# Kernel tuning notes

Measured on AMD Instinct MI355X. Metric: run time of the kernel, lower is better.

The kernel has to match this reference:

```python
import jax, jax.numpy as jnp
import numpy as np

B, V, D, H, E = 512, 128, 256, 4, 2
Dh = D // H

def setup_inputs() -> dict:
    key = jax.random.key(0)
    k = jax.random.split(key, 8)
    x = jax.random.normal(k[0], (B, V, D), dtype=jnp.float32)
    adj = jax.random.randint(k[1], (V, V), 0, 2, dtype=jnp.int32)
    adj = adj.at[jnp.arange(V), jnp.arange(V)].set(1)  # self loops so no empty columns for real nodes
    edge_attr = jax.random.normal(k[2], (V, V, E), dtype=jnp.float32)
    mask = jax.random.bernoulli(k[3], 0.1, (B, V))  # True = padded view
    # learned params (torch Linear: y = x @ W.T)
    W = jax.random.normal(k[4], (D, D), dtype=jnp.float32) / np.sqrt(D)
    a = jax.random.normal(k[5], (2 * Dh,), dtype=jnp.float32) / np.sqrt(2 * Dh)  # attn.weight flattened
    Ew = jax.random.normal(k[6], (H, E), dtype=jnp.float32) / np.sqrt(E)  # edge_proj.weight
    return {"x": x, "adj": adj, "edge_attr": edge_attr, "mask": mask, "W": W, "a": a, "Ew": Ew}

def reference(x, adj, edge_attr, mask, W, a, Ew):
    Bv, Vv, Dv = x.shape
    Hh = Ew.shape[0]
    Dhh = Dv // Hh
    Wx = (x @ W.T).reshape(Bv, Vv, Hh, Dhh)                 # [B,V,H,Dh]
    a_src, a_dst = a[:Dhh], a[Dhh:]
    s_src = jnp.einsum('bvhd,d->bvh', Wx, a_src)             # a^T[Wh_i ; .]
    s_dst = jnp.einsum('bvhd,d->bvh', Wx, a_dst)             # a^T[. ; Wh_j]
    ef = jnp.einsum('ije,he->ijh', edge_attr, Ew)            # [V,V,H]
    e = s_src[:, :, None, :] + s_dst[:, None, :, :] + ef[None]  # [B,i,j,H]
    e = jnp.where(e >= 0, e, 0.2 * e)                        # leaky_relu(0.2)
    valid = (adj.astype(bool))[None, :, :, None] & (~mask)[:, :, None, None] & (~mask)[:, None, :, None]
    e = jnp.where(valid, e, -jnp.inf)
    # softmax over source dim i (axis=1), safe for all-masked columns (-> 0, like nan_to_num)
    m = jnp.max(e, axis=1, keepdims=True)
    m = jnp.where(jnp.isfinite(m), m, 0.0)
    p = jnp.where(valid, jnp.exp(e - m), 0.0)
    denom = jnp.sum(p, axis=1, keepdims=True)
    alpha = p / jnp.where(denom == 0, 1.0, denom)            # [B,i,j,H]
    h = jnp.einsum('bijh,bihd->bjhd', alpha, Wx).reshape(Bv, Vv, Dv)
    h = jax.nn.elu(h)
    return jnp.where(mask[:, :, None], 0.0, h)
```

## Files before the change

### kernel.cpp

```cpp
#include <hip/hip_runtime.h>
#include <hip/hip_bf16.h>
#include <cmath>

#define BB 512
#define VV 128
#define DD 256
#define HH 4
#define DHH 64

typedef unsigned short u16;
typedef __attribute__((ext_vector_type(8))) short bf16x8;
typedef __attribute__((ext_vector_type(4))) float f32x4;

__device__ __forceinline__ unsigned pk2(float a, float b) {
    __hip_bfloat162 h = __float22bfloat162_rn(make_float2(a, b));
    unsigned r;
    __builtin_memcpy(&r, &h, sizeof(r));
    return r;
}

__global__ __launch_bounds__(256) void k_ef(const float* __restrict__ ea,
                                            const float* __restrict__ Ew,
                                            const int* __restrict__ adj,
                                            float* __restrict__ efmT) {
    __shared__ float tile[32][33];
    const int jt = blockIdx.x, it = blockIdx.y, h = blockIdx.z;
    const int t = threadIdx.x;
    const float e0 = Ew[h * 2], e1 = Ew[h * 2 + 1];
    const int jl = t & 31, il = t >> 5;
    #pragma unroll
    for (int p = 0; p < 4; ++p) {
        const int i = it * 32 + p * 8 + il;
        const int j = jt * 32 + jl;
        const int ij = i * VV + j;
        float v = -INFINITY;
        if (adj[ij]) v = fmaf(ea[ij * 2 + 1], e1, ea[ij * 2] * e0);
        tile[p * 8 + il][jl] = v;
    }
    __syncthreads();
    const int i2 = t & 31, j2 = t >> 5;
    #pragma unroll
    for (int p = 0; p < 4; ++p) {
        const int j = p * 8 + j2;
        efmT[((size_t)h * VV + jt * 32 + j) * VV + it * 32 + i2] = tile[i2][j];
    }
}

__global__ __launch_bounds__(256, 3) void k_fused(
    const float* __restrict__ x, const float* __restrict__ Wm,
    const float* __restrict__ a, const float* __restrict__ efmT,
    const int* __restrict__ mask, float* __restrict__ out) {
    __shared__ u16 WxL[128 * 136];
    __shared__ float ssl[256], sdl[256], rden[2][128];

    const int t = threadIdx.x;
    const int b = blockIdx.x, hp = blockIdx.y;
    const int w = t >> 6, L = t & 63;
    const int wr = w >> 1, wc = w & 1;
    const int lr = L & 15, lg = L >> 4;

    const float* xb = x  + ((size_t)b * VV + wr * 64 + lr) * DD + lg * 8;
    const float* wb = Wm + ((size_t)(hp * 128 + wc * 64 + lr)) * DD + lg * 8;

    f32x4 acc[4][4];
    #pragma unroll
    for (int i = 0; i < 4; ++i)
        #pragma unroll
        for (int j = 0; j < 4; ++j) acc[i][j] = (f32x4){0.f, 0.f, 0.f, 0.f};

    for (int ks = 0; ks < 8; ++ks) {
        float4 la[4][2], lb[4][2];
        #pragma unroll
        for (int f = 0; f < 4; ++f) {
            la[f][0] = *(const float4*)(xb + (size_t)f * 16 * DD + ks * 32);
            la[f][1] = *(const float4*)(xb + (size_t)f * 16 * DD + ks * 32 + 4);
        }
        #pragma unroll
        for (int f = 0; f < 4; ++f) {
            lb[f][0] = *(const float4*)(wb + (size_t)f * 16 * DD + ks * 32);
            lb[f][1] = *(const float4*)(wb + (size_t)f * 16 * DD + ks * 32 + 4);
        }
        bf16x8 af[4], bf[4];
        #pragma unroll
        for (int f = 0; f < 4; ++f) {
            unsigned* u = (unsigned*)&af[f];
            u[0] = pk2(la[f][0].x, la[f][0].y); u[1] = pk2(la[f][0].z, la[f][0].w);
            u[2] = pk2(la[f][1].x, la[f][1].y); u[3] = pk2(la[f][1].z, la[f][1].w);
            unsigned* v = (unsigned*)&bf[f];
            v[0] = pk2(lb[f][0].x, lb[f][0].y); v[1] = pk2(lb[f][0].z, lb[f][0].w);
            v[2] = pk2(lb[f][1].x, lb[f][1].y); v[3] = pk2(lb[f][1].z, lb[f][1].w);
        }
        #pragma unroll
        for (int mi = 0; mi < 4; ++mi)
            #pragma unroll
            for (int ni = 0; ni < 4; ++ni)
                acc[mi][ni] = __builtin_amdgcn_mfma_f32_16x16x32_bf16(
                    af[mi], bf[ni], acc[mi][ni], 0, 0, 0);
    }

    float as_[4], ad_[4];
    #pragma unroll
    for (int ni = 0; ni < 4; ++ni) {
        as_[ni] = a[ni * 16 + lr];
        ad_[ni] = a[64 + ni * 16 + lr];
    }
    float ps[16], pd[16];
    #pragma unroll
    for (int k = 0; k < 16; ++k) { ps[k] = 0.f; pd[k] = 0.f; }
    #pragma unroll
    for (int mi = 0; mi < 4; ++mi) {
        #pragma unroll
        for (int ni = 0; ni < 4; ++ni) {
            const int c  = wc * 64 + ni * 16 + lr;
            const int vb = wr * 64 + mi * 16 + lg * 4;
            unsigned o2[2];
            o2[0] = pk2(acc[mi][ni][0], acc[mi][ni][1]);
            o2[1] = pk2(acc[mi][ni][2], acc[mi][ni][3]);
            #pragma unroll
            for (int r = 0; r < 4; ++r) {
                float v = acc[mi][ni][r];
                ps[mi * 4 + r] = fmaf(v, as_[ni], ps[mi * 4 + r]);
                pd[mi * 4 + r] = fmaf(v, ad_[ni], pd[mi * 4 + r]);
            }
            *(uint2*)&WxL[c * 136 + vb] = *(uint2*)&o2[0];
        }
    }
    #pragma unroll
    for (int k = 0; k < 16; ++k) {
        #pragma unroll
        for (int m = 1; m < 16; m <<= 1) {
            ps[k] += __shfl_xor(ps[k], m);
            pd[k] += __shfl_xor(pd[k], m);
        }
    }
    if (lr == 0) {
        #pragma unroll
        for (int mi = 0; mi < 4; ++mi)
            #pragma unroll
            for (int r = 0; r < 4; ++r) {
                int v = wr * 64 + mi * 16 + lg * 4 + r;
                bool mk = mask[b * VV + v] != 0;
                ssl[wc * 128 + v] = mk ? -INFINITY : ps[mi * 4 + r];
                sdl[wc * 128 + v] = mk ? -INFINITY : pd[mi * 4 + r];
            }
    }
    __syncthreads();

    const int j0 = w * 32 + lr;
    for (int hl = 0; hl < 2; ++hl) {
        const int h = hp * 2 + hl;
        const float sdj0 = sdl[hl * 128 + j0];
        const float sdj1 = sdl[hl * 128 + j0 + 16];
        const float* ef0 = efmT + ((size_t)h * VV + j0) * VV;
        const float* ef1 = ef0 + 16 * VV;
        bf16x8 af2[2][4];
        float ps0 = 0.f, ps1 = 0.f;
        #pragma unroll
        for (int ks = 0; ks < 4; ++ks) {
            const int i0 = ks * 32 + lg * 8;
            float sv[8], ev0[8], ev1[8];
            *(float4*)&sv[0]  = *(const float4*)&ssl[hl * 128 + i0];
            *(float4*)&sv[4]  = *(const float4*)&ssl[hl * 128 + i0 + 4];
            *(float4*)&ev0[0] = *(const float4*)(ef0 + i0);
            *(float4*)&ev0[4] = *(const float4*)(ef0 + i0 + 4);
            *(float4*)&ev1[0] = *(const float4*)(ef1 + i0);
            *(float4*)&ev1[4] = *(const float4*)(ef1 + i0 + 4);
            float p0[8], p1[8];
            #pragma unroll
            for (int u = 0; u < 8; ++u) {
                float e0 = sv[u] + sdj0 + ev0[u];
                float e1 = sv[u] + sdj1 + ev1[u];
                e0 = fmaxf(e0, 0.2f * e0);
                e1 = fmaxf(e1, 0.2f * e1);
                p0[u] = __expf(e0); ps0 += p0[u];
                p1[u] = __expf(e1); ps1 += p1[u];
            }
            unsigned* a0 = (unsigned*)&af2[0][ks];
            unsigned* a1 = (unsigned*)&af2[1][ks];
            a0[0] = pk2(p0[0], p0[1]); a0[1] = pk2(p0[2], p0[3]);
            a0[2] = pk2(p0[4], p0[5]); a0[3] = pk2(p0[6], p0[7]);
            a1[0] = pk2(p1[0], p1[1]); a1[1] = pk2(p1[2], p1[3]);
            a1[2] = pk2(p1[4], p1[5]); a1[3] = pk2(p1[6], p1[7]);
        }
        ps0 += __shfl_xor(ps0, 16); ps0 += __shfl_xor(ps0, 32);
        ps1 += __shfl_xor(ps1, 16); ps1 += __shfl_xor(ps1, 32);
        if (lg == 0) {
            rden[hl][j0]      = ps0 > 0.f ? 1.f / ps0 : 0.f;
            rden[hl][j0 + 16] = ps1 > 0.f ? 1.f / ps1 : 0.f;
        }

        f32x4 acc2[2][4];
        #pragma unroll
        for (int mi = 0; mi < 2; ++mi)
            #pragma unroll
            for (int ni = 0; ni < 4; ++ni) acc2[mi][ni] = (f32x4){0.f, 0.f, 0.f, 0.f};
        #pragma unroll
        for (int ks = 0; ks < 4; ++ks) {
            const int kk = ks * 32 + lg * 8;
            #pragma unroll
            for (int ni = 0; ni < 4; ++ni) {
                bf16x8 bf2 = *(const bf16x8*)&WxL[(hl * 64 + ni * 16 + lr) * 136 + kk];
                acc2[0][ni] = __builtin_amdgcn_mfma_f32_16x16x32_bf16(
                    af2[0][ks], bf2, acc2[0][ni], 0, 0, 0);
                acc2[1][ni] = __builtin_amdgcn_mfma_f32_16x16x32_bf16(
                    af2[1][ks], bf2, acc2[1][ni], 0, 0, 0);
            }
        }

        #pragma unroll
        for (int mi = 0; mi < 2; ++mi)
            #pragma unroll
            for (int ni = 0; ni < 4; ++ni) {
                const int dcol = ni * 16 + lr;
                const int jb   = w * 32 + mi * 16 + lg * 4;
                float* op = out + ((size_t)b * VV + jb) * DD + h * DHH + dcol;
                #pragma unroll
                for (int r = 0; r < 4; ++r) {
                    float v = acc2[mi][ni][r] * rden[hl][jb + r];
                    v = v > 0.f ? v : (__expf(v) - 1.0f);
                    op[(size_t)r * DD] = v;
                }
            }
    }
}

extern "C" void kernel_launch(void* const* d_in, const int* in_sizes, int n_in,
                              void* d_out, int out_size, void* d_ws, size_t ws_size,
                              hipStream_t stream) {
    const float* x    = (const float*)d_in[0];
    const int*   adj  = (const int*)d_in[1];
    const float* ea   = (const float*)d_in[2];
    const int*   mask = (const int*)d_in[3];
    const float* Wm   = (const float*)d_in[4];
    const float* a    = (const float*)d_in[5];
    const float* Ew   = (const float*)d_in[6];
    float* out = (float*)d_out;

    float* efmT = (float*)d_ws;

    k_ef<<<dim3(4, 4, HH), 256, 0, stream>>>(ea, Ew, adj, efmT);
    k_fused<<<dim3(BB, 2), 256, 0, stream>>>(x, Wm, a, efmT, mask, out);
}
```

Baseline: 182.8 us.

## Split fused GAT kernel per head and stage GEMM operands through LDS

```diff
diff --git a/kernel.cpp b/kernel.cpp
--- a/kernel.cpp
+++ b/kernel.cpp
@@ -46,56 +46,75 @@
     }
 }
 
-__global__ __launch_bounds__(256, 3) void k_fused(
+__global__ __launch_bounds__(256, 4) void k_fused(
     const float* __restrict__ x, const float* __restrict__ Wm,
     const float* __restrict__ a, const float* __restrict__ efmT,
     const int* __restrict__ mask, float* __restrict__ out) {
-    __shared__ u16 WxL[128 * 136];
-    __shared__ float ssl[256], sdl[256], rden[2][128];
+    __shared__ u16 ubuf[8704];
+    __shared__ float ssl[128], sdl[128], rden[128];
+
+    u16* As  = ubuf;
+    u16* Bs  = ubuf + 5120;
+    u16* WxL = ubuf;
 
     const int t = threadIdx.x;
-    const int b = blockIdx.x, hp = blockIdx.y;
+    const int h = blockIdx.x, b = blockIdx.y;
     const int w = t >> 6, L = t & 63;
-    const int wr = w >> 1, wc = w & 1;
     const int lr = L & 15, lg = L >> 4;
 
-    const float* xb = x  + ((size_t)b * VV + wr * 64 + lr) * DD + lg * 8;
-    const float* wb = Wm + ((size_t)(hp * 128 + wc * 64 + lr)) * DD + lg * 8;
-
-    f32x4 acc[4][4];
-    #pragma unroll
-    for (int i = 0; i < 4; ++i)
+    const int arow = t >> 1, aseg = t & 1;
+    const int brow = t >> 2, bseg = t & 3;
+    const float* xs = x  + ((size_t)b * VV + arow) * DD + aseg * 16;
+    const float* ws = Wm + ((size_t)(h * 64 + brow)) * DD + bseg * 8;
+    u16* adst = As + arow * 40 + aseg * 16;
+    u16* bdst = Bs + brow * 40 + bseg * 8;
+
+    f32x4 acc[2][4];
+    #pragma unroll
+    for (int i = 0; i < 2; ++i)
         #pragma unroll
         for (int j = 0; j < 4; ++j) acc[i][j] = (f32x4){0.f, 0.f, 0.f, 0.f};
 
+    float4 px[4], pw[2];
+    #pragma unroll
+    for (int q = 0; q < 4; ++q) px[q] = *(const float4*)(xs + q * 4);
+    #pragma unroll
+    for (int q = 0; q < 2; ++q) pw[q] = *(const float4*)(ws + q * 4);
+
     for (int ks = 0; ks < 8; ++ks) {
-        float4 la[4][2], lb[4][2];
-        #pragma unroll
-        for (int f = 0; f < 4; ++f) {
-            la[f][0] = *(const float4*)(xb + (size_t)f * 16 * DD + ks * 32);
-            la[f][1] = *(const float4*)(xb + (size_t)f * 16 * DD + ks * 32 + 4);
-        }
-        #pragma unroll
-        for (int f = 0; f < 4; ++f) {
-            lb[f][0] = *(const float4*)(wb + (size_t)f * 16 * DD + ks * 32);
-            lb[f][1] = *(const float4*)(wb + (size_t)f * 16 * DD + ks * 32 + 4);
-        }
-        bf16x8 af[4], bf[4];
-        #pragma unroll
-        for (int f = 0; f < 4; ++f) {
-            unsigned* u = (unsigned*)&af[f];
-            u[0] = pk2(la[f][0].x, la[f][0].y); u[1] = pk2(la[f][0].z, la[f][0].w);
-            u[2] = pk2(la[f][1].x, la[f][1].y); u[3] = pk2(la[f][1].z, la[f][1].w);
-            unsigned* v = (unsigned*)&bf[f];
-            v[0] = pk2(lb[f][0].x, lb[f][0].y); v[1] = pk2(lb[f][0].z, lb[f][0].w);
-            v[2] = pk2(lb[f][1].x, lb[f][1].y); v[3] = pk2(lb[f][1].z, lb[f][1].w);
-        }
-        #pragma unroll
-        for (int mi = 0; mi < 4; ++mi)
+        unsigned va[4], vb[4], qa[4];
+        va[0] = pk2(px[0].x, px[0].y); va[1] = pk2(px[0].z, px[0].w);
+        va[2] = pk2(px[1].x, px[1].y); va[3] = pk2(px[1].z, px[1].w);
+        vb[0] = pk2(px[2].x, px[2].y); vb[1] = pk2(px[2].z, px[2].w);
+        vb[2] = pk2(px[3].x, px[3].y); vb[3] = pk2(px[3].z, px[3].w);
+        qa[0] = pk2(pw[0].x, pw[0].y); qa[1] = pk2(pw[0].z, pw[0].w);
+        qa[2] = pk2(pw[1].x, pw[1].y); qa[3] = pk2(pw[1].z, pw[1].w);
+        *(bf16x8*)adst       = *(bf16x8*)&va[0];
+        *(bf16x8*)(adst + 8) = *(bf16x8*)&vb[0];
+        *(bf16x8*)bdst       = *(bf16x8*)&qa[0];
+        __syncthreads();
+        if (ks < 7) {
+            #pragma unroll
+            for (int q = 0; q < 4; ++q)
+                px[q] = *(const float4*)(xs + (ks + 1) * 32 + q * 4);
+            #pragma unroll
+            for (int q = 0; q < 2; ++q)
+                pw[q] = *(const float4*)(ws + (ks + 1) * 32 + q * 4);
+        }
+        bf16x8 af[2], bfr[4];
+        #pragma unroll
+        for (int mi = 0; mi < 2; ++mi)
+            af[mi] = *(const bf16x8*)&As[(w * 32 + mi * 16 + lr) * 40 + lg * 8];
+        #pragma unroll
+        for (int ni = 0; ni < 4; ++ni)
+            bfr[ni] = *(const bf16x8*)&Bs[(ni * 16 + lr) * 40 + lg * 8];
+        #pragma unroll
+        for (int mi = 0; mi < 2; ++mi)
             #pragma unroll
             for (int ni = 0; ni < 4; ++ni)
                 acc[mi][ni] = __builtin_amdgcn_mfma_f32_16x16x32_bf16(
-                    af[mi], bf[ni], acc[mi][ni], 0, 0, 0);
+                    af[mi], bfr[ni], acc[mi][ni], 0, 0, 0);
+        __syncthreads();
     }
 
     float as_[4], ad_[4];
@@ -104,15 +123,15 @@
         as_[ni] = a[ni * 16 + lr];
         ad_[ni] = a[64 + ni * 16 + lr];
     }
-    float ps[16], pd[16];
-    #pragma unroll
-    for (int k = 0; k < 16; ++k) { ps[k] = 0.f; pd[k] = 0.f; }
-    #pragma unroll
-    for (int mi = 0; mi < 4; ++mi) {
+    float ps[8], pd[8];
+    #pragma unroll
+    for (int k = 0; k < 8; ++k) { ps[k] = 0.f; pd[k] = 0.f; }
+    #pragma unroll
+    for (int mi = 0; mi < 2; ++mi) {
         #pragma unroll
         for (int ni = 0; ni < 4; ++ni) {
-            const int c  = wc * 64 + ni * 16 + lr;
-            const int vb = wr * 64 + mi * 16 + lg * 4;
+            const int c  = ni * 16 + lr;
+            const int vb = w * 32 + mi * 16 + lg * 4;
             unsigned o2[2];
             o2[0] = pk2(acc[mi][ni][0], acc[mi][ni][1]);
             o2[1] = pk2(acc[mi][ni][2], acc[mi][ni][3]);
@@ -126,7 +145,7 @@
         }
     }
     #pragma unroll
-    for (int k = 0; k < 16; ++k) {
+    for (int k = 0; k < 8; ++k) {
         #pragma unroll
         for (int m = 1; m < 16; m <<= 1) {
             ps[k] += __shfl_xor(ps[k], m);
@@ -135,93 +154,90 @@
     }
     if (lr == 0) {
         #pragma unroll
-        for (int mi = 0; mi < 4; ++mi)
+        for (int mi = 0; mi < 2; ++mi)
             #pragma unroll
             for (int r = 0; r < 4; ++r) {
-                int v = wr * 64 + mi * 16 + lg * 4 + r;
+                int v = w * 32 + mi * 16 + lg * 4 + r;
                 bool mk = mask[b * VV + v] != 0;
-                ssl[wc * 128 + v] = mk ? -INFINITY : ps[mi * 4 + r];
-                sdl[wc * 128 + v] = mk ? -INFINITY : pd[mi * 4 + r];
+                ssl[v] = mk ? -INFINITY : ps[mi * 4 + r];
+                sdl[v] = mk ? -INFINITY : pd[mi * 4 + r];
             }
     }
     __syncthreads();
 
     const int j0 = w * 32 + lr;
-    for (int hl = 0; hl < 2; ++hl) {
-        const int h = hp * 2 + hl;
-        const float sdj0 = sdl[hl * 128 + j0];
-        const float sdj1 = sdl[hl * 128 + j0 + 16];
-        const float* ef0 = efmT + ((size_t)h * VV + j0) * VV;
-        const float* ef1 = ef0 + 16 * VV;
-        bf16x8 af2[2][4];
-        float ps0 = 0.f, ps1 = 0.f;
-        #pragma unroll
-        for (int ks = 0; ks < 4; ++ks) {
-            const int i0 = ks * 32 + lg * 8;
-            float sv[8], ev0[8], ev1[8];
-            *(float4*)&sv[0]  = *(const float4*)&ssl[hl * 128 + i0];
-            *(float4*)&sv[4]  = *(const float4*)&ssl[hl * 128 + i0 + 4];
-            *(float4*)&ev0[0] = *(const float4*)(ef0 + i0);
-            *(float4*)&ev0[4] = *(const float4*)(ef0 + i0 + 4);
-            *(float4*)&ev1[0] = *(const float4*)(ef1 + i0);
-            *(float4*)&ev1[4] = *(const float4*)(ef1 + i0 + 4);
-            float p0[8], p1[8];
-            #pragma unroll
-            for (int u = 0; u < 8; ++u) {
-                float e0 = sv[u] + sdj0 + ev0[u];
-                float e1 = sv[u] + sdj1 + ev1[u];
-                e0 = fmaxf(e0, 0.2f * e0);
-                e1 = fmaxf(e1, 0.2f * e1);
-                p0[u] = __expf(e0); ps0 += p0[u];
-                p1[u] = __expf(e1); ps1 += p1[u];
+    const float sdj0 = sdl[j0];
+    const float sdj1 = sdl[j0 + 16];
+    const float* ef0 = efmT + ((size_t)h * VV + j0) * VV;
+    const float* ef1 = ef0 + 16 * VV;
+    bf16x8 af2[2][4];
+    float ps0 = 0.f, ps1 = 0.f;
+    #pragma unroll
+    for (int ks = 0; ks < 4; ++ks) {
+        const int i0 = ks * 32 + lg * 8;
+        float sv[8], ev0[8], ev1[8];
+        *(float4*)&sv[0]  = *(const float4*)&ssl[i0];
+        *(float4*)&sv[4]  = *(const float4*)&ssl[i0 + 4];
+        *(float4*)&ev0[0] = *(const float4*)(ef0 + i0);
+        *(float4*)&ev0[4] = *(const float4*)(ef0 + i0 + 4);
+        *(float4*)&ev1[0] = *(const float4*)(ef1 + i0);
+        *(float4*)&ev1[4] = *(const float4*)(ef1 + i0 + 4);
+        float p0[8], p1[8];
+        #pragma unroll
+        for (int u = 0; u < 8; ++u) {
+            float e0 = sv[u] + sdj0 + ev0[u];
+            float e1 = sv[u] + sdj1 + ev1[u];
+            e0 = fmaxf(e0, 0.2f * e0);
+            e1 = fmaxf(e1, 0.2f * e1);
+            p0[u] = __expf(e0); ps0 += p0[u];
+            p1[u] = __expf(e1); ps1 += p1[u];
+        }
+        unsigned* a0 = (unsigned*)&af2[0][ks];
+        unsigned* a1 = (unsigned*)&af2[1][ks];
+        a0[0] = pk2(p0[0], p0[1]); a0[1] = pk2(p0[2], p0[3]);
+        a0[2] = pk2(p0[4], p0[5]); a0[3] = pk2(p0[6], p0[7]);
+        a1[0] = pk2(p1[0], p1[1]); a1[1] = pk2(p1[2], p1[3]);
+        a1[2] = pk2(p1[4], p1[5]); a1[3] = pk2(p1[6], p1[7]);
+    }
+    ps0 += __shfl_xor(ps0, 16); ps0 += __shfl_xor(ps0, 32);
+    ps1 += __shfl_xor(ps1, 16); ps1 += __shfl_xor(ps1, 32);
+    if (lg == 0) {
+        rden[j0]      = ps0 > 0.f ? 1.f / ps0 : 0.f;
+        rden[j0 + 16] = ps1 > 0.f ? 1.f / ps1 : 0.f;
+    }
+
+    f32x4 acc2[2][4];
+    #pragma unroll
+    for (int mi = 0; mi < 2; ++mi)
+        #pragma unroll
+        for (int ni = 0; ni < 4; ++ni) acc2[mi][ni] = (f32x4){0.f, 0.f, 0.f, 0.f};
+    #pragma unroll
+    for (int ks = 0; ks < 4; ++ks) {
+        const int kk = ks * 32 + lg * 8;
+        #pragma unroll
+        for (int ni = 0; ni < 4; ++ni) {
+            bf16x8 bf2 = *(const bf16x8*)&WxL[(ni * 16 + lr) * 136 + kk];
+            acc2[0][ni] = __builtin_amdgcn_mfma_f32_16x16x32_bf16(
+                af2[0][ks], bf2, acc2[0][ni], 0, 0, 0);
+            acc2[1][ni] = __builtin_amdgcn_mfma_f32_16x16x32_bf16(
+                af2[1][ks], bf2, acc2[1][ni], 0, 0, 0);
+        }
+    }
+
+    #pragma unroll
+    for (int mi = 0; mi < 2; ++mi)
+        #pragma unroll
+        for (int ni = 0; ni < 4; ++ni) {
+            const int dcol = ni * 16 + lr;
+            const int jb   = w * 32 + mi * 16 + lg * 4;
+            float* op = out + ((size_t)b * VV + jb) * DD + h * DHH + dcol;
+            #pragma unroll
+            for (int r = 0; r < 4; ++r) {
+                float v = acc2[mi][ni][r] * rden[jb + r];
+                v = v > 0.f ? v : (__expf(v) - 1.0f);
+                op[(size_t)r * DD] = v;
             }
-            unsigned* a0 = (unsigned*)&af2[0][ks];
-            unsigned* a1 = (unsigned*)&af2[1][ks];
-            a0[0] = pk2(p0[0], p0[1]); a0[1] = pk2(p0[2], p0[3]);
-            a0[2] = pk2(p0[4], p0[5]); a0[3] = pk2(p0[6], p0[7]);
-            a1[0] = pk2(p1[0], p1[1]); a1[1] = pk2(p1[2], p1[3]);
-            a1[2] = pk2(p1[4], p1[5]); a1[3] = pk2(p1[6], p1[7]);
-        }
-        ps0 += __shfl_xor(ps0, 16); ps0 += __shfl_xor(ps0, 32);
-        ps1 += __shfl_xor(ps1, 16); ps1 += __shfl_xor(ps1, 32);
-        if (lg == 0) {
-            rden[hl][j0]      = ps0 > 0.f ? 1.f / ps0 : 0.f;
-            rden[hl][j0 + 16] = ps1 > 0.f ? 1.f / ps1 : 0.f;
-        }
-
-        f32x4 acc2[2][4];
-        #pragma unroll
-        for (int mi = 0; mi < 2; ++mi)
-            #pragma unroll
-            for (int ni = 0; ni < 4; ++ni) acc2[mi][ni] = (f32x4){0.f, 0.f, 0.f, 0.f};
-        #pragma unroll
-        for (int ks = 0; ks < 4; ++ks) {
-            const int kk = ks * 32 + lg * 8;
-            #pragma unroll
-            for (int ni = 0; ni < 4; ++ni) {
-                bf16x8 bf2 = *(const bf16x8*)&WxL[(hl * 64 + ni * 16 + lr) * 136 + kk];
-                acc2[0][ni] = __builtin_amdgcn_mfma_f32_16x16x32_bf16(
-                    af2[0][ks], bf2, acc2[0][ni], 0, 0, 0);
-                acc2[1][ni] = __builtin_amdgcn_mfma_f32_16x16x32_bf16(
-                    af2[1][ks], bf2, acc2[1][ni], 0, 0, 0);
-            }
-        }
-
-        #pragma unroll
-        for (int mi = 0; mi < 2; ++mi)
-            #pragma unroll
-            for (int ni = 0; ni < 4; ++ni) {
-                const int dcol = ni * 16 + lr;
-                const int jb   = w * 32 + mi * 16 + lg * 4;
-                float* op = out + ((size_t)b * VV + jb) * DD + h * DHH + dcol;
-                #pragma unroll
-                for (int r = 0; r < 4; ++r) {
-                    float v = acc2[mi][ni][r] * rden[hl][jb + r];
-                    v = v > 0.f ? v : (__expf(v) - 1.0f);
-                    op[(size_t)r * DD] = v;
-                }
-            }
-    }
+        }
 }
 
 extern "C" void kernel_launch(void* const* d_in, const int* in_sizes, int n_in,
@@ -239,5 +255,5 @@
     float* efmT = (float*)d_ws;
 
     k_ef<<<dim3(4, 4, HH), 256, 0, stream>>>(ea, Ew, adj, efmT);
-    k_fused<<<dim3(BB, 2), 256, 0, stream>>>(x, Wm, a, efmT, mask, out);
-}
+    k_fused<<<dim3(HH, BB), 256, 0, stream>>>(x, Wm, a, efmT, mask, out);
+}
```

New measurement: 171.6 us. 6.1% less time.

## Stage GEMM operands through LDS via direct global-to-LDS loads with swizzle

Applied to the files above, without the earlier changes.

```diff
diff --git a/kernel.cpp b/kernel.cpp
--- a/kernel.cpp
+++ b/kernel.cpp
@@ -17,6 +17,12 @@
     unsigned r;
     __builtin_memcpy(&r, &h, sizeof(r));
     return r;
+}
+
+__device__ __forceinline__ void gld16(const float* g, float* lds) {
+    __builtin_amdgcn_global_load_lds(
+        (const __attribute__((address_space(1))) void*)g,
+        (__attribute__((address_space(3))) void*)lds, 16, 0, 0);
 }
 
 __global__ __launch_bounds__(256) void k_ef(const float* __restrict__ ea,
@@ -46,12 +52,16 @@
     }
 }
 
-__global__ __launch_bounds__(256, 3) void k_fused(
+__global__ __launch_bounds__(256, 4) void k_fused(
     const float* __restrict__ x, const float* __restrict__ Wm,
     const float* __restrict__ a, const float* __restrict__ efmT,
     const int* __restrict__ mask, float* __restrict__ out) {
-    __shared__ u16 WxL[128 * 136];
+    __shared__ __align__(16) char ubuf[34816];
+    float* As  = (float*)ubuf;
+    float* Bsf = As + 4096;
+    u16*   WxL = (u16*)ubuf;
     __shared__ float ssl[256], sdl[256], rden[2][128];
+    __shared__ int mkl[128];
 
     const int t = threadIdx.x;
     const int b = blockIdx.x, hp = blockIdx.y;
@@ -59,8 +69,14 @@
     const int wr = w >> 1, wc = w & 1;
     const int lr = L & 15, lg = L >> 4;
 
-    const float* xb = x  + ((size_t)b * VV + wr * 64 + lr) * DD + lg * 8;
-    const float* wb = Wm + ((size_t)(hp * 128 + wc * 64 + lr)) * DD + lg * 8;
+    if (t < 128) mkl[t] = mask[b * VV + t];
+
+    const int lrow = L >> 3;
+    const int scol = ((L & 7) ^ (lrow & 7)) * 4;
+    const float* gA = x  + ((size_t)b * VV + w * 8 + lrow) * DD + scol;
+    const float* gB = Wm + ((size_t)(hp * 128 + w * 8 + lrow)) * DD + scol;
+    float* ldsA = As  + w * 256;
+    float* ldsB = Bsf + w * 256;
 
     f32x4 acc[4][4];
     #pragma unroll
@@ -69,33 +85,39 @@
         for (int j = 0; j < 4; ++j) acc[i][j] = (f32x4){0.f, 0.f, 0.f, 0.f};
 
     for (int ks = 0; ks < 8; ++ks) {
-        float4 la[4][2], lb[4][2];
-        #pragma unroll
-        for (int f = 0; f < 4; ++f) {
-            la[f][0] = *(const float4*)(xb + (size_t)f * 16 * DD + ks * 32);
-            la[f][1] = *(const float4*)(xb + (size_t)f * 16 * DD + ks * 32 + 4);
-        }
-        #pragma unroll
-        for (int f = 0; f < 4; ++f) {
-            lb[f][0] = *(const float4*)(wb + (size_t)f * 16 * DD + ks * 32);
-            lb[f][1] = *(const float4*)(wb + (size_t)f * 16 * DD + ks * 32 + 4);
-        }
-        bf16x8 af[4], bf[4];
-        #pragma unroll
-        for (int f = 0; f < 4; ++f) {
-            unsigned* u = (unsigned*)&af[f];
-            u[0] = pk2(la[f][0].x, la[f][0].y); u[1] = pk2(la[f][0].z, la[f][0].w);
-            u[2] = pk2(la[f][1].x, la[f][1].y); u[3] = pk2(la[f][1].z, la[f][1].w);
-            unsigned* v = (unsigned*)&bf[f];
-            v[0] = pk2(lb[f][0].x, lb[f][0].y); v[1] = pk2(lb[f][0].z, lb[f][0].w);
-            v[2] = pk2(lb[f][1].x, lb[f][1].y); v[3] = pk2(lb[f][1].z, lb[f][1].w);
+        #pragma unroll
+        for (int r = 0; r < 4; ++r) {
+            gld16(gA + r * 8192 + ks * 32, ldsA + r * 1024);
+            gld16(gB + r * 8192 + ks * 32, ldsB + r * 1024);
+        }
+        __syncthreads();
+        const int sw = (lr & 7) << 2;
+        bf16x8 af[4], bfr[4];
+        #pragma unroll
+        for (int mi = 0; mi < 4; ++mi) {
+            const float* rp = As + (wr * 64 + mi * 16 + lr) * 32;
+            float4 f0 = *(const float4*)&rp[(lg * 8) ^ sw];
+            float4 f1 = *(const float4*)&rp[(lg * 8 + 4) ^ sw];
+            unsigned* u = (unsigned*)&af[mi];
+            u[0] = pk2(f0.x, f0.y); u[1] = pk2(f0.z, f0.w);
+            u[2] = pk2(f1.x, f1.y); u[3] = pk2(f1.z, f1.w);
+        }
+        #pragma unroll
+        for (int ni = 0; ni < 4; ++ni) {
+            const float* rp = Bsf + (wc * 64 + ni * 16 + lr) * 32;
+            float4 f0 = *(const float4*)&rp[(lg * 8) ^ sw];
+            float4 f1 = *(const float4*)&rp[(lg * 8 + 4) ^ sw];
+            unsigned* u = (unsigned*)&bfr[ni];
+            u[0] = pk2(f0.x, f0.y); u[1] = pk2(f0.z, f0.w);
+            u[2] = pk2(f1.x, f1.y); u[3] = pk2(f1.z, f1.w);
         }
         #pragma unroll
         for (int mi = 0; mi < 4; ++mi)
             #pragma unroll
             for (int ni = 0; ni < 4; ++ni)
                 acc[mi][ni] = __builtin_amdgcn_mfma_f32_16x16x32_bf16(
-                    af[mi], bf[ni], acc[mi][ni], 0, 0, 0);
+                    af[mi], bfr[ni], acc[mi][ni], 0, 0, 0);
+        __syncthreads();
     }
 
     float as_[4], ad_[4];
@@ -139,7 +161,7 @@
             #pragma unroll
             for (int r = 0; r < 4; ++r) {
                 int v = wr * 64 + mi * 16 + lg * 4 + r;
-                bool mk = mask[b * VV + v] != 0;
+                bool mk = mkl[v] != 0;
                 ssl[wc * 128 + v] = mk ? -INFINITY : ps[mi * 4 + r];
                 sdl[wc * 128 + v] = mk ? -INFINITY : pd[mi * 4 + r];
             }
```

New measurement: 149.1 us. 1.23x faster.
